# Kernel tuning notes

Hardware: AMD Instinct MI355X
Metric: run time of the kernel (lower is better)

Reference implementation:

```python
import jax, jax.numpy as jnp
import numpy as np

N_NODES = 100000
N_EDGES = 1600000
NUM_GRAPHS = 64
IN_CH, HID, NUM_CLASSES = 128, 64, 10


def _glorot(key, fan_in, fan_out):
    scale = jnp.sqrt(2.0 / (fan_in + fan_out)).astype(jnp.float32)
    return jax.random.normal(key, (fan_in, fan_out), jnp.float32) * scale


def setup_inputs() -> dict:
    key = jax.random.key(0)
    ks = jax.random.split(key, 7)
    x = jax.random.normal(ks[0], (N_NODES, IN_CH), jnp.float32)
    edge_index = jax.random.randint(ks[1], (2, N_EDGES), 0, N_NODES, dtype=jnp.int32)
    batch = jnp.sort(jax.random.randint(ks[2], (N_NODES,), 0, NUM_GRAPHS, dtype=jnp.int32))
    return {
        "x": x,
        "edge_index": edge_index,
        "batch": batch,
        "W1": _glorot(ks[3], IN_CH, HID), "b1": jnp.zeros((HID,), jnp.float32),
        "W2": _glorot(ks[4], HID, HID), "b2": jnp.zeros((HID,), jnp.float32),
        "W3": _glorot(ks[5], HID, NUM_CLASSES), "b3": jnp.zeros((NUM_CLASSES,), jnp.float32),
    }


def _gcn_conv(x, src, dst, norm, W, b):
    # GCNConv: h = X W, then symmetric-normalized scatter-add over edges, then + b
    h = x @ W                                  # [N, out]
    msg = norm[:, None] * h[src]               # [E+N, out] gather
    out = jax.ops.segment_sum(msg, dst, num_segments=N_NODES)
    return out + b


def reference(x, edge_index, batch, W1, b1, W2, b2, W3, b3):
    loop = jnp.arange(N_NODES, dtype=edge_index.dtype)
    src = jnp.concatenate([edge_index[0], loop])   # self-loops added (PyG gcn_norm)
    dst = jnp.concatenate([edge_index[1], loop])
    deg = jax.ops.segment_sum(jnp.ones(src.shape[0], x.dtype), dst, num_segments=N_NODES)
    dinv = jnp.where(deg > 0, jax.lax.rsqrt(deg), jnp.zeros_like(deg))
    norm = dinv[src] * dinv[dst]

    h = jax.nn.relu(_gcn_conv(x, src, dst, norm, W1, b1))  # dropout is identity in eval
    h = jax.nn.relu(_gcn_conv(h, src, dst, norm, W2, b2))
    h = _gcn_conv(h, src, dst, norm, W3, b3)

    counts = jax.ops.segment_sum(jnp.ones(N_NODES, h.dtype), batch, num_segments=NUM_GRAPHS)
    pooled = jax.ops.segment_sum(h, batch, num_segments=NUM_GRAPHS) / jnp.maximum(counts, 1.0)[:, None]
    return jax.nn.log_softmax(pooled, axis=1)
```

## Files before the change

### kernel.cpp

```cpp
#include <hip/hip_runtime.h>
#include <math.h>

#define IN_CH 128
#define HID   64
#define NC    10
#define BSH   8
#define NBLK  256

typedef unsigned short bfu;
typedef __attribute__((ext_vector_type(8))) short bf16x8;
typedef __attribute__((ext_vector_type(4))) float f32x4;
typedef __attribute__((ext_vector_type(2))) float f32x2;

static __device__ __forceinline__ bfu bf16_of(float f) {
    unsigned u = __float_as_uint(f);
    unsigned r = (u + 0x7FFF + ((u >> 16) & 1)) >> 16;
    return (bfu)r;
}

#if __has_builtin(__builtin_amdgcn_cvt_pk_f32_fp8) && __has_builtin(__builtin_amdgcn_cvt_pk_fp8_f32)
template <bool HI>
static __device__ __forceinline__ f32x2 fp8_unpk(unsigned d) {
    return __builtin_amdgcn_cvt_pk_f32_fp8((int)d, HI);
}
template <bool HI>
static __device__ __forceinline__ int fp8_pk(float a, float b, int old) {
    return __builtin_amdgcn_cvt_pk_fp8_f32(a, b, old, HI);
}
#else
static __device__ __forceinline__ float fp8_dec1(unsigned b) {
    unsigned s = b >> 7, e = (b >> 3) & 15, m = b & 7;
    float v = (e == 0) ? ldexpf((float)m, -9) : ldexpf((float)(8 + m), (int)e - 10);
    return s ? -v : v;
}
static __device__ __forceinline__ unsigned fp8_enc1(float f) {
    unsigned u = __float_as_uint(f);
    unsigned s = (u >> 31) << 7;
    f = fabsf(f);
    if (!(f < 448.f)) return s | 0x7E;
    if (f < 0.015625f) {
        int q = (int)rintf(f * 512.f);
        return s | (unsigned)q;
    }
    int e; float fr = frexpf(f, &e);
    int q = (int)rintf(fr * 16.f);
    if (q == 16) { q = 8; e++; }
    int E = e + 6;
    if (E >= 16) return s | 0x7E;
    return s | (unsigned)((E << 3) | (q - 8));
}
template <bool HI>
static __device__ __forceinline__ f32x2 fp8_unpk(unsigned d) {
    unsigned w = HI ? (d >> 16) : d;
    f32x2 r; r.x = fp8_dec1(w & 0xFF); r.y = fp8_dec1((w >> 8) & 0xFF);
    return r;
}
template <bool HI>
static __device__ __forceinline__ int fp8_pk(float a, float b, int old) {
    unsigned p = fp8_enc1(a) | (fp8_enc1(b) << 8);
    return HI ? (int)(((unsigned)old & 0x0000FFFFu) | (p << 16))
              : (int)(((unsigned)old & 0xFFFF0000u) | p);
}
#endif

__device__ __forceinline__ int lower_bound_i(const int* a, int n, int v) {
    int lo = 0, hi = n;
    while (lo < hi) { int mid = (lo + hi) >> 1; if (a[mid] < v) lo = mid + 1; else hi = mid; }
    return lo;
}


__global__ void k_init(int* __restrict__ cnt, float* __restrict__ Psum,
                       unsigned* __restrict__ dumA, unsigned* __restrict__ dumB,
                       const float* __restrict__ W1, const float* __restrict__ W2,
                       bfu* __restrict__ W1b, bfu* __restrict__ W2b,
                       int nbuck, int ng) {
    int t = threadIdx.x, b = blockIdx.x;
    if (b == 0) {
        for (int i = t; i < nbuck; i += 256) cnt[i] = 0;
        if (t < 16) { dumA[t] = 0u; dumB[t] = 0u; }
    } else if (b == 1) {
        for (int i = t; i < ng * HID; i += 256) Psum[i] = 0.f;
    } else if (b < 6) {
        int base = (b - 2) * 2048;
        for (int i = t; i < 2048; i += 256) {
            int idx = base + i;
            int k = idx >> 6, c = idx & 63;
            W1b[c * 136 + k] = bf16_of(W1[idx]);
        }
    } else {
        int base = (b - 6) * 2048;
        for (int i = t; i < 2048; i += 256) {
            int idx = base + i;
            int k = idx >> 6, c = idx & 63;
            W2b[c * 72 + k] = bf16_of(W2[idx]);
        }
    }
}


__global__ __launch_bounds__(1024) void k_part(const int* __restrict__ src,
                                               const int* __restrict__ dst,
                                               int* __restrict__ cnt,
                                               unsigned* __restrict__ packed,
                                               int E, int nbuck, int chunk, int cap) {
    __shared__ int hist[512];
    int tid = threadIdx.x;
    for (int b = tid; b < nbuck; b += 1024) hist[b] = 0;
    __syncthreads();
    int base = blockIdx.x * chunk;
    int lim  = min(base + chunk, E);
    for (int e = base + tid; e < lim; e += 1024)
        atomicAdd(&hist[dst[e] >> BSH], 1);
    __syncthreads();
    for (int b = tid; b < nbuck; b += 1024) {
        int c = hist[b];
        hist[b] = c ? atomicAdd(&cnt[b], c) : 0;
    }
    __syncthreads();
    for (int e = base + tid; e < lim; e += 1024) {
        int d = dst[e], s = src[e];
        int b = d >> BSH;
        int pos = atomicAdd(&hist[b], 1);
        if (pos < cap)
            packed[(size_t)b * (size_t)cap + pos] = ((unsigned)s << 8) | (unsigned)(d & 255);
    }
}


__global__ __launch_bounds__(1024) void k_placeC(const unsigned* __restrict__ packed,
                                                 const int* __restrict__ cnt,
                                                 int2* __restrict__ rp2,
                                                 float* __restrict__ dinv,
                                                 int* __restrict__ meta,
                                                 int nn, int cap, int capm) {
    __shared__ int hist[256];
    __shared__ int scn[256];
    __shared__ int cur[256];
    int tid = threadIdx.x;
    int b   = blockIdx.x;
    int nb0 = b << BSH;
    int nnb = min(1 << BSH, nn - nb0);
    if (tid < 256) hist[tid] = 0;
    __syncthreads();
    int lo = b * cap;
    int hi = lo + min(cnt[b], cap);
    for (int e = lo + tid; e < hi; e += blockDim.x)
        atomicAdd(&hist[packed[e] & 255u], 1);
    __syncthreads();
    int pd = 0;
    if (tid < 256) { pd = (hist[tid] + 3) & ~3; scn[tid] = pd; }
    __syncthreads();
    for (int off = 1; off < 256; off <<= 1) {
        int t = 0;
        if (tid < 256 && tid >= off) t = scn[tid - off];
        __syncthreads();
        if (tid < 256) scn[tid] += t;
        __syncthreads();
    }
    int meta0 = b * capm;
    if (tid < nnb) {
        int rp = meta0 + scn[tid] - pd;
        rp2[nb0 + tid] = make_int2(rp, rp + pd);
        cur[tid] = rp;
        dinv[nb0 + tid] = rsqrtf((float)(hist[tid] + 1));
        for (int k = hist[tid]; k < pd; k++) meta[rp + k] = nn;
    }
    __syncthreads();
    for (int e = lo + tid; e < hi; e += blockDim.x) {
        unsigned p = packed[e];
        int pos = atomicAdd(&cur[p & 255u], 1);
        meta[pos] = (int)(p >> 8);
    }
}


template <int K, bool IN_BF16>
__global__ __launch_bounds__(256) void k_gemm(const void* __restrict__ Xv,
                                              const bfu* __restrict__ Wb,
                                              const float* __restrict__ dinv,
                                              unsigned char* __restrict__ G8, int n) {
    constexpr int KS = K + 8;
    __shared__ bfu wt[64 * KS];
    int tid = threadIdx.x;
    {
        const uint4* wsrc = (const uint4*)Wb;
        uint4* wdst = (uint4*)wt;
        for (int i = tid; i < 8 * KS; i += 256) wdst[i] = wsrc[i];
    }
    __syncthreads();
    int wave = tid >> 6, lane = tid & 63;
    int m = lane & 15, q = lane >> 4;
    int row0 = blockIdx.x * 64 + wave * 16;
    int rowA = min(row0 + m, n - 1);
    f32x4 acc[4] = {{0.f,0.f,0.f,0.f},{0.f,0.f,0.f,0.f},
                    {0.f,0.f,0.f,0.f},{0.f,0.f,0.f,0.f}};
#pragma unroll
    for (int ks = 0; ks < K / 32; ks++) {
        bf16x8 a;
        if (IN_BF16) {
            a = *(const bf16x8*)((const bfu*)Xv + (size_t)rowA * 64 + ks * 32 + q * 8);
        } else {
            const float* xp = (const float*)Xv + (size_t)rowA * K + ks * 32 + q * 8;
            float4 v0 = *(const float4*)xp;
            float4 v1 = *(const float4*)(xp + 4);
            union { unsigned u[4]; bf16x8 v; } cvt;
            cvt.u[0] = __builtin_amdgcn_perm(__float_as_uint(v0.y), __float_as_uint(v0.x), 0x07060302u);
            cvt.u[1] = __builtin_amdgcn_perm(__float_as_uint(v0.w), __float_as_uint(v0.z), 0x07060302u);
            cvt.u[2] = __builtin_amdgcn_perm(__float_as_uint(v1.y), __float_as_uint(v1.x), 0x07060302u);
            cvt.u[3] = __builtin_amdgcn_perm(__float_as_uint(v1.w), __float_as_uint(v1.z), 0x07060302u);
            a = cvt.v;
        }
#pragma unroll
        for (int nt = 0; nt < 4; nt++) {
            bf16x8 b = *(const bf16x8*)&wt[(nt * 16 + m) * KS + ks * 32 + q * 8];
            acc[nt] = __builtin_amdgcn_mfma_f32_16x16x32_bf16(a, b, acc[nt], 0, 0, 0);
        }
    }
#pragma unroll
    for (int r = 0; r < 4; r++) {
        int grow = row0 + q * 4 + r;
        if (grow < n) {
            float dv = dinv[grow];
            int p01 = fp8_pk<false>(acc[0][r] * dv, acc[1][r] * dv, 0);
            int p23 = fp8_pk<false>(acc[2][r] * dv, acc[3][r] * dv, 0);
            unsigned char* gp = G8 + (size_t)grow * 64 + m;
            gp[0]  = (unsigned char)(p01 & 0xFF);
            gp[16] = (unsigned char)((p01 >> 8) & 0xFF);
            gp[32] = (unsigned char)(p23 & 0xFF);
            gp[48] = (unsigned char)((p23 >> 8) & 0xFF);
        }
    }
}


template <int MODE>
__global__ void k_agg(const unsigned* __restrict__ G4, const int* __restrict__ meta,
                      const int2* __restrict__ rp2, const float* __restrict__ dinv,
                      const float* __restrict__ bias, void* __restrict__ outv,
                      const int* __restrict__ batch, float* __restrict__ Psum,
                      const bfu* __restrict__ Wb,
                      int n, int ng, int do_relu, int post_scale) {
    extern __shared__ char smem[];
    int tid = threadIdx.x;
    if (MODE == 3) {
        bfu* wt = (bfu*)(smem + 16 * 72 * 2);
        const uint4* wsrc = (const uint4*)Wb;
        uint4* wdst = (uint4*)wt;
        for (int i = tid; i < 576; i += 256) wdst[i] = wsrc[i];
    }
    int wbase = ((blockIdx.x * blockDim.x + tid) >> 6) * 4;
    if (MODE == 1) { if (wbase >= n) return; }
    int lane = tid & 63;
    int col4 = lane & 15, equad = lane >> 4;
    int nb0 = blockIdx.x * 16;
    if (MODE == 2 && tid < 16) {
        int* sb = (int*)(smem + 16 * 64 * 4);
        sb[tid] = (nb0 + tid < n) ? batch[nb0 + tid] : -1;
    }
    int nd    = wbase + equad;
    bool alive = nd < n;
    int ndc   = alive ? nd : (n - 1);
    int2 rp = rp2[ndc];
    int beg = rp.x, pend = alive ? rp.y : rp.x;
    unsigned sv = G4[(size_t)ndc * 16 + col4];
    float dv = dinv[ndc];
    f32x2 aA = {0.f, 0.f}, aB = {0.f, 0.f};
    int e = beg;
    for (; e + 8 <= pend; e += 8) {
        int4 m0 = *(const int4*)&meta[e];
        int4 m1 = *(const int4*)&meta[e + 4];
        unsigned d0 = G4[(size_t)m0.x * 16 + col4];
        unsigned d1 = G4[(size_t)m0.y * 16 + col4];
        unsigned d2 = G4[(size_t)m0.z * 16 + col4];
        unsigned d3 = G4[(size_t)m0.w * 16 + col4];
        unsigned d4 = G4[(size_t)m1.x * 16 + col4];
        unsigned d5 = G4[(size_t)m1.y * 16 + col4];
        unsigned d6 = G4[(size_t)m1.z * 16 + col4];
        unsigned d7 = G4[(size_t)m1.w * 16 + col4];
        aA += fp8_unpk<false>(d0); aB += fp8_unpk<true>(d0);
        aA += fp8_unpk<false>(d1); aB += fp8_unpk<true>(d1);
        aA += fp8_unpk<false>(d2); aB += fp8_unpk<true>(d2);
        aA += fp8_unpk<false>(d3); aB += fp8_unpk<true>(d3);
        aA += fp8_unpk<false>(d4); aB += fp8_unpk<true>(d4);
        aA += fp8_unpk<false>(d5); aB += fp8_unpk<true>(d5);
        aA += fp8_unpk<false>(d6); aB += fp8_unpk<true>(d6);
        aA += fp8_unpk<false>(d7); aB += fp8_unpk<true>(d7);
    }
    if (e < pend) {
        int4 m = *(const int4*)&meta[e];
        unsigned d0 = G4[(size_t)m.x * 16 + col4];
        unsigned d1 = G4[(size_t)m.y * 16 + col4];
        unsigned d2 = G4[(size_t)m.z * 16 + col4];
        unsigned d3 = G4[(size_t)m.w * 16 + col4];
        aA += fp8_unpk<false>(d0); aB += fp8_unpk<true>(d0);
        aA += fp8_unpk<false>(d1); aB += fp8_unpk<true>(d1);
        aA += fp8_unpk<false>(d2); aB += fp8_unpk<true>(d2);
        aA += fp8_unpk<false>(d3); aB += fp8_unpk<true>(d3);
    }
    aA += fp8_unpk<false>(sv); aB += fp8_unpk<true>(sv);
    float a0 = aA.x * dv, a1 = aA.y * dv, a2 = aB.x * dv, a3 = aB.y * dv;
    if (bias) {
        float4 bv = *(const float4*)&bias[col4 * 4];
        a0 += bv.x; a1 += bv.y; a2 += bv.z; a3 += bv.w;
    }
    if (do_relu) {
        a0 = fmaxf(a0, 0.f); a1 = fmaxf(a1, 0.f);
        a2 = fmaxf(a2, 0.f); a3 = fmaxf(a3, 0.f);
    }
    if (post_scale) { a0 *= dv; a1 *= dv; a2 *= dv; a3 *= dv; }
    if (MODE == 3) {
        bfu* pw = (bfu*)smem;
        bfu* wt = (bfu*)(smem + 16 * 72 * 2);
        int slot = (tid >> 6) * 4 + equad;
        uint2 o;
        o.x = (unsigned)bf16_of(alive ? a0 : 0.f) | ((unsigned)bf16_of(alive ? a1 : 0.f) << 16);
        o.y = (unsigned)bf16_of(alive ? a2 : 0.f) | ((unsigned)bf16_of(alive ? a3 : 0.f) << 16);
        *(uint2*)&pw[slot * 72 + col4 * 4] = o;
        __syncthreads();
        int w = tid >> 6, m = col4, q = equad;
        f32x4 acc = {0.f, 0.f, 0.f, 0.f};
#pragma unroll
        for (int ks = 0; ks < 2; ks++) {
            bf16x8 av = *(const bf16x8*)&pw[m * 72 + ks * 32 + q * 8];
            bf16x8 bv = *(const bf16x8*)&wt[(w * 16 + m) * 72 + ks * 32 + q * 8];
            acc = __builtin_amdgcn_mfma_f32_16x16x32_bf16(av, bv, acc, 0, 0, 0);
        }
        int c = w * 16 + m;
        int r0 = nb0 + q * 4;
        float dv0 = dinv[min(r0 + 0, n - 1)], dv1 = dinv[min(r0 + 1, n - 1)];
        float dv2 = dinv[min(r0 + 2, n - 1)], dv3 = dinv[min(r0 + 3, n - 1)];
        int p01 = fp8_pk<false>(acc[0] * dv0, acc[1] * dv1, 0);
        int p23 = fp8_pk<false>(acc[2] * dv2, acc[3] * dv3, 0);
        unsigned char* gp = (unsigned char*)outv;
        if (r0 + 0 < n) gp[(size_t)(r0 + 0) * 64 + c] = (unsigned char)(p01 & 0xFF);
        if (r0 + 1 < n) gp[(size_t)(r0 + 1) * 64 + c] = (unsigned char)((p01 >> 8) & 0xFF);
        if (r0 + 2 < n) gp[(size_t)(r0 + 2) * 64 + c] = (unsigned char)(p23 & 0xFF);
        if (r0 + 3 < n) gp[(size_t)(r0 + 3) * 64 + c] = (unsigned char)((p23 >> 8) & 0xFF);
    } else if (MODE == 2) {
        float* pwf = (float*)smem;
        int*   sb  = (int*)(smem + 16 * 64 * 4);
        int slot = (tid >> 6) * 4 + equad;
        f32x4 st;
        st.x = alive ? a0 : 0.f; st.y = alive ? a1 : 0.f;
        st.z = alive ? a2 : 0.f; st.w = alive ? a3 : 0.f;
        *(f32x4*)&pwf[slot * 64 + col4 * 4] = st;
        __syncthreads();
        int r = tid >> 6, cc = tid & 63;
        int g0 = sb[0];
        float v = 0.f;
#pragma unroll
        for (int s2 = 0; s2 < 16; s2++)
            if (sb[s2] == g0 + r) v += pwf[s2 * 64 + cc];
        if (v != 0.f && g0 + r < ng) atomicAdd(&Psum[(g0 + r) * 64 + cc], v);
        if (tid < 16) {
            int bb = sb[tid];
            if (bb > g0 + 3) {
                for (int c2 = 0; c2 < 64; c2++)
                    atomicAdd(&Psum[bb * 64 + c2], pwf[tid * 64 + c2]);
            }
        }
    } else if (alive) {
        int p = fp8_pk<false>(a0, a1, 0);
        p = fp8_pk<true>(a2, a3, p);
        ((unsigned*)outv)[(size_t)nd * 16 + col4] = (unsigned)p;
    }
}


__global__ void k_final(const float* __restrict__ Psum, const int* __restrict__ batch,
                        int n, const float* __restrict__ W3, const float* __restrict__ b3,
                        float* __restrict__ out, int ng) {
    __shared__ float P[64 * 64];
    __shared__ float s[64][NC];
    __shared__ float lse[64];
    __shared__ float invc[64];
    int t = threadIdx.x;
    if (t < ng) {
        int lo = lower_bound_i(batch, n, t);
        int hi = lower_bound_i(batch, n, t + 1);
        invc[t] = 1.f / (float)max(hi - lo, 1);
    }
    __syncthreads();
    for (int i = t; i < ng * 64; i += blockDim.x) P[i] = Psum[i] * invc[i >> 6];
    __syncthreads();
    if (t < ng * NC) {
        int g = t / NC, c = t % NC;
        float acc = b3[c];
        for (int k = 0; k < 64; k++) acc += P[g * 64 + k] * W3[k * NC + c];
        s[g][c] = acc;
    }
    __syncthreads();
    if (t < ng) {
        float m = -1e30f;
        for (int c = 0; c < NC; c++) m = fmaxf(m, s[t][c]);
        float sum = 0.f;
        for (int c = 0; c < NC; c++) sum += expf(s[t][c] - m);
        lse[t] = m + logf(sum);
    }
    __syncthreads();
    if (t < ng * NC) {
        int g = t / NC, c = t % NC;
        out[t] = s[g][c] - lse[g];
    }
}


extern "C" void kernel_launch(void* const* d_in, const int* in_sizes, int n_in,
                              void* d_out, int out_size, void* d_ws, size_t ws_size,
                              hipStream_t stream) {
    const float* x     = (const float*)d_in[0];
    const int*   ei    = (const int*)  d_in[1];
    const int*   batch = (const int*)  d_in[2];
    const float* W1    = (const float*)d_in[3];
    const float* b1    = (const float*)d_in[4];
    const float* W2    = (const float*)d_in[5];
    const float* b2    = (const float*)d_in[6];
    const float* W3    = (const float*)d_in[7];
    const float* b3    = (const float*)d_in[8];
    float*       out   = (float*)d_out;

    const int NN = in_sizes[0] / IN_CH;
    const int E  = in_sizes[1] / 2;
    const int NG = out_size / NC;
    const int nbuck = (NN + (1 << BSH) - 1) >> BSH;
    const int cap   = (int)(((((long long)E << BSH) / NN) + 768 + 3) & ~3LL);
    const int capm  = cap + 772;

    const int* src = ei;
    const int* dst = ei + E;

    char* ws = (char*)d_ws;
    size_t off = 0;
    auto carve = [&](size_t bytes) -> char* {
        char* p = ws + off;
        off = (off + bytes + 255) & ~(size_t)255;
        return p;
    };
    int2*  rp2    = (int2*) carve((size_t)NN * 8);
    float* dinv   = (float*)carve((size_t)NN * 4);
    int*   cnt    = (int*)  carve((size_t)nbuck * 4);
    int*   meta   = (int*)  carve(((size_t)nbuck * capm + 64) * 4);
    unsigned char* f8A = (unsigned char*)carve((size_t)(NN + 1) * 64);
    unsigned char* f8B = (unsigned char*)carve((size_t)(NN + 1) * 64);
    unsigned* packed = (unsigned*)carve((size_t)nbuck * cap * 4);
    float* Psum   = (float*)carve((size_t)NG * HID * 4);
    bfu*   W1b    = (bfu*)  carve((size_t)64 * 136 * 2);
    bfu*   W2b    = (bfu*)  carve((size_t)64 * 72 * 2);
    (void)ws_size;

    const int chnk = (E + NBLK - 1) / NBLK;
    const int nbG  = (NN + 63) / 64;
    const int nbA  = (NN + 15) / 16;

    const int smem3 = (16 * 72 + 64 * 72) * 2;
    const int smem2 = 16 * 64 * 4 + 16 * 4;

    k_init<<<8, 256, 0, stream>>>(cnt, Psum,
                                  (unsigned*)(f8A + (size_t)NN * 64),
                                  (unsigned*)(f8B + (size_t)NN * 64),
                                  W1, W2, W1b, W2b, nbuck, NG);
    k_part<<<NBLK, 1024, 0, stream>>>(src, dst, cnt, packed, E, nbuck, chnk, cap);
    k_placeC<<<nbuck, 1024, 0, stream>>>(packed, cnt, rp2, dinv, meta, NN, cap, capm);

    k_gemm<IN_CH, false><<<nbG, 256, 0, stream>>>(x, W1b, dinv, f8A, NN);
    k_agg<3><<<nbA, 256, smem3, stream>>>((const unsigned*)f8A, meta, rp2, dinv, b1,
                                          f8B, nullptr, nullptr, W2b, NN, NG, 1, 0);
    k_agg<1><<<nbA, 256, 0, stream>>>((const unsigned*)f8B, meta, rp2, dinv, b2,
                                      f8A, nullptr, nullptr, nullptr, NN, NG, 1, 1);
    k_agg<2><<<nbA, 256, smem2, stream>>>((const unsigned*)f8A, meta, rp2, dinv, nullptr,
                                          nullptr, batch, Psum, nullptr, NN, NG, 0, 0);
    k_final<<<1, 640, 0, stream>>>(Psum, batch, NN, W3, b3, out, NG);
}
```

Before: 232.5 us.

## Count degrees in partition pass and fuse final pooling head into last aggregation

Per-node in-degrees are now counted with global atomics during the edge partition pass, so the placement kernel no longer makes a separate histogram pass over the packed edges. The standalone final kernel is removed. Its work (mean pooling, the W3 projection and log_softmax) now runs in the last block of the final aggregation kernel, chosen with a completion counter and a thread fence, which saves one launch. The cost is 1.6M extra global atomics on random addresses in the partition pass, plus a larger shared-memory footprint for the last aggregation kernel.

```diff
diff --git a/kernel.cpp b/kernel.cpp
--- a/kernel.cpp
+++ b/kernel.cpp
@@ -74,10 +74,11 @@
                        unsigned* __restrict__ dumA, unsigned* __restrict__ dumB,
                        const float* __restrict__ W1, const float* __restrict__ W2,
                        bfu* __restrict__ W1b, bfu* __restrict__ W2b,
-                       int nbuck, int ng) {
+                       int* __restrict__ deg, int nn, int nbuck, int ng) {
     int t = threadIdx.x, b = blockIdx.x;
+    for (int i = b * 256 + t; i < nn; i += 8 * 256) deg[i] = 0;
     if (b == 0) {
-        for (int i = t; i < nbuck; i += 256) cnt[i] = 0;
+        for (int i = t; i < nbuck + 1; i += 256) cnt[i] = 0;
         if (t < 16) { dumA[t] = 0u; dumB[t] = 0u; }
     } else if (b == 1) {
         for (int i = t; i < ng * HID; i += 256) Psum[i] = 0.f;
@@ -102,6 +103,7 @@
 __global__ __launch_bounds__(1024) void k_part(const int* __restrict__ src,
                                                const int* __restrict__ dst,
                                                int* __restrict__ cnt,
+                                               int* __restrict__ deg,
                                                unsigned* __restrict__ packed,
                                                int E, int nbuck, int chunk, int cap) {
     __shared__ int hist[512];
@@ -110,8 +112,11 @@
     __syncthreads();
     int base = blockIdx.x * chunk;
     int lim  = min(base + chunk, E);
-    for (int e = base + tid; e < lim; e += 1024)
-        atomicAdd(&hist[dst[e] >> BSH], 1);
+    for (int e = base + tid; e < lim; e += 1024) {
+        int d = dst[e];
+        atomicAdd(&hist[d >> BSH], 1);
+        atomicAdd(&deg[d], 1);
+    }
     __syncthreads();
     for (int b = tid; b < nbuck; b += 1024) {
         int c = hist[b];
@@ -130,26 +135,23 @@
 
 __global__ __launch_bounds__(1024) void k_placeC(const unsigned* __restrict__ packed,
                                                  const int* __restrict__ cnt,
+                                                 const int* __restrict__ deg,
                                                  int2* __restrict__ rp2,
                                                  float* __restrict__ dinv,
                                                  int* __restrict__ meta,
                                                  int nn, int cap, int capm) {
-    __shared__ int hist[256];
     __shared__ int scn[256];
     __shared__ int cur[256];
     int tid = threadIdx.x;
     int b   = blockIdx.x;
     int nb0 = b << BSH;
     int nnb = min(1 << BSH, nn - nb0);
-    if (tid < 256) hist[tid] = 0;
-    __syncthreads();
-    int lo = b * cap;
-    int hi = lo + min(cnt[b], cap);
-    for (int e = lo + tid; e < hi; e += blockDim.x)
-        atomicAdd(&hist[packed[e] & 255u], 1);
-    __syncthreads();
-    int pd = 0;
-    if (tid < 256) { pd = (hist[tid] + 3) & ~3; scn[tid] = pd; }
+    int dg = 0, pd = 0;
+    if (tid < 256) {
+        dg = (tid < nnb) ? deg[nb0 + tid] : 0;
+        pd = (dg + 3) & ~3;
+        scn[tid] = pd;
+    }
     __syncthreads();
     for (int off = 1; off < 256; off <<= 1) {
         int t = 0;
@@ -163,10 +165,12 @@
         int rp = meta0 + scn[tid] - pd;
         rp2[nb0 + tid] = make_int2(rp, rp + pd);
         cur[tid] = rp;
-        dinv[nb0 + tid] = rsqrtf((float)(hist[tid] + 1));
-        for (int k = hist[tid]; k < pd; k++) meta[rp + k] = nn;
-    }
-    __syncthreads();
+        dinv[nb0 + tid] = rsqrtf((float)(dg + 1));
+        for (int k = dg; k < pd; k++) meta[rp + k] = nn;
+    }
+    __syncthreads();
+    int lo = b * cap;
+    int hi = lo + min(cnt[b], cap);
     for (int e = lo + tid; e < hi; e += blockDim.x) {
         unsigned p = packed[e];
         int pos = atomicAdd(&cur[p & 255u], 1);
@@ -240,6 +244,8 @@
                       const float* __restrict__ bias, void* __restrict__ outv,
                       const int* __restrict__ batch, float* __restrict__ Psum,
                       const bfu* __restrict__ Wb,
+                      const float* __restrict__ W3, const float* __restrict__ b3,
+                      float* __restrict__ outp, int* __restrict__ donecnt,
                       int n, int ng, int do_relu, int post_scale) {
     extern __shared__ char smem[];
     int tid = threadIdx.x;
@@ -255,7 +261,7 @@
     int col4 = lane & 15, equad = lane >> 4;
     int nb0 = blockIdx.x * 16;
     if (MODE == 2 && tid < 16) {
-        int* sb = (int*)(smem + 16 * 64 * 4);
+        int* sb = (int*)(smem + 19456);
         sb[tid] = (nb0 + tid < n) ? batch[nb0 + tid] : -1;
     }
     int nd    = wbase + equad;
@@ -339,7 +345,7 @@
         if (r0 + 3 < n) gp[(size_t)(r0 + 3) * 64 + c] = (unsigned char)((p23 >> 8) & 0xFF);
     } else if (MODE == 2) {
         float* pwf = (float*)smem;
-        int*   sb  = (int*)(smem + 16 * 64 * 4);
+        int*   sb  = (int*)(smem + 19456);
         int slot = (tid >> 6) * 4 + equad;
         f32x4 st;
         st.x = alive ? a0 : 0.f; st.y = alive ? a1 : 0.f;
@@ -360,48 +366,50 @@
                     atomicAdd(&Psum[bb * 64 + c2], pwf[tid * 64 + c2]);
             }
         }
+        __threadfence();
+        __shared__ int lastf;
+        if (tid == 0) {
+            int rk = atomicAdd(donecnt, 1);
+            lastf = (rk == (int)gridDim.x - 1) ? 1 : 0;
+        }
+        __syncthreads();
+        if (lastf) {
+            float* P    = (float*)smem;
+            float* sS   = (float*)(smem + 16384);
+            float* lse  = (float*)(smem + 18944);
+            float* invc = (float*)(smem + 19200);
+            if (tid < ng) {
+                int lo2 = lower_bound_i(batch, n, tid);
+                int hi2 = lower_bound_i(batch, n, tid + 1);
+                invc[tid] = 1.f / (float)max(hi2 - lo2, 1);
+            }
+            __syncthreads();
+            for (int i = tid; i < ng * 64; i += 256)
+                P[i] = __hip_atomic_load(&Psum[i], __ATOMIC_RELAXED,
+                                         __HIP_MEMORY_SCOPE_AGENT) * invc[i >> 6];
+            __syncthreads();
+            for (int idx = tid; idx < ng * NC; idx += 256) {
+                int g = idx / NC, c = idx % NC;
+                float acc2 = b3[c];
+                for (int k = 0; k < 64; k++) acc2 += P[g * 64 + k] * W3[k * NC + c];
+                sS[idx] = acc2;
+            }
+            __syncthreads();
+            if (tid < ng) {
+                float mx = -1e30f;
+                for (int c = 0; c < NC; c++) mx = fmaxf(mx, sS[tid * NC + c]);
+                float sum = 0.f;
+                for (int c = 0; c < NC; c++) sum += expf(sS[tid * NC + c] - mx);
+                lse[tid] = mx + logf(sum);
+            }
+            __syncthreads();
+            for (int idx = tid; idx < ng * NC; idx += 256)
+                outp[idx] = sS[idx] - lse[idx / NC];
+        }
     } else if (alive) {
         int p = fp8_pk<false>(a0, a1, 0);
         p = fp8_pk<true>(a2, a3, p);
         ((unsigned*)outv)[(size_t)nd * 16 + col4] = (unsigned)p;
-    }
-}
-
-
-__global__ void k_final(const float* __restrict__ Psum, const int* __restrict__ batch,
-                        int n, const float* __restrict__ W3, const float* __restrict__ b3,
-                        float* __restrict__ out, int ng) {
-    __shared__ float P[64 * 64];
-    __shared__ float s[64][NC];
-    __shared__ float lse[64];
-    __shared__ float invc[64];
-    int t = threadIdx.x;
-    if (t < ng) {
-        int lo = lower_bound_i(batch, n, t);
-        int hi = lower_bound_i(batch, n, t + 1);
-        invc[t] = 1.f / (float)max(hi - lo, 1);
-    }
-    __syncthreads();
-    for (int i = t; i < ng * 64; i += blockDim.x) P[i] = Psum[i] * invc[i >> 6];
-    __syncthreads();
-    if (t < ng * NC) {
-        int g = t / NC, c = t % NC;
-        float acc = b3[c];
-        for (int k = 0; k < 64; k++) acc += P[g * 64 + k] * W3[k * NC + c];
-        s[g][c] = acc;
-    }
-    __syncthreads();
-    if (t < ng) {
-        float m = -1e30f;
-        for (int c = 0; c < NC; c++) m = fmaxf(m, s[t][c]);
-        float sum = 0.f;
-        for (int c = 0; c < NC; c++) sum += expf(s[t][c] - m);
-        lse[t] = m + logf(sum);
-    }
-    __syncthreads();
-    if (t < ng * NC) {
-        int g = t / NC, c = t % NC;
-        out[t] = s[g][c] - lse[g];
     }
 }
 
@@ -439,7 +447,8 @@
     };
     int2*  rp2    = (int2*) carve((size_t)NN * 8);
     float* dinv   = (float*)carve((size_t)NN * 4);
-    int*   cnt    = (int*)  carve((size_t)nbuck * 4);
+    int*   cnt    = (int*)  carve((size_t)(nbuck + 1) * 4);
+    int*   deg    = (int*)  carve((size_t)NN * 4);
     int*   meta   = (int*)  carve(((size_t)nbuck * capm + 64) * 4);
     unsigned char* f8A = (unsigned char*)carve((size_t)(NN + 1) * 64);
     unsigned char* f8B = (unsigned char*)carve((size_t)(NN + 1) * 64);
@@ -448,27 +457,30 @@
     bfu*   W1b    = (bfu*)  carve((size_t)64 * 136 * 2);
     bfu*   W2b    = (bfu*)  carve((size_t)64 * 72 * 2);
     (void)ws_size;
+    int* donecnt = cnt + nbuck;
 
     const int chnk = (E + NBLK - 1) / NBLK;
     const int nbG  = (NN + 63) / 64;
     const int nbA  = (NN + 15) / 16;
 
     const int smem3 = (16 * 72 + 64 * 72) * 2;
-    const int smem2 = 16 * 64 * 4 + 16 * 4;
+    const int smem2 = 19520;
 
     k_init<<<8, 256, 0, stream>>>(cnt, Psum,
                                   (unsigned*)(f8A + (size_t)NN * 64),
                                   (unsigned*)(f8B + (size_t)NN * 64),
-                                  W1, W2, W1b, W2b, nbuck, NG);
-    k_part<<<NBLK, 1024, 0, stream>>>(src, dst, cnt, packed, E, nbuck, chnk, cap);
-    k_placeC<<<nbuck, 1024, 0, stream>>>(packed, cnt, rp2, dinv, meta, NN, cap, capm);
+                                  W1, W2, W1b, W2b, deg, NN, nbuck, NG);
+    k_part<<<NBLK, 1024, 0, stream>>>(src, dst, cnt, deg, packed, E, nbuck, chnk, cap);
+    k_placeC<<<nbuck, 1024, 0, stream>>>(packed, cnt, deg, rp2, dinv, meta, NN, cap, capm);
 
     k_gemm<IN_CH, false><<<nbG, 256, 0, stream>>>(x, W1b, dinv, f8A, NN);
     k_agg<3><<<nbA, 256, smem3, stream>>>((const unsigned*)f8A, meta, rp2, dinv, b1,
-                                          f8B, nullptr, nullptr, W2b, NN, NG, 1, 0);
+                                          f8B, nullptr, nullptr, W2b,
+                                          nullptr, nullptr, nullptr, nullptr, NN, NG, 1, 0);
     k_agg<1><<<nbA, 256, 0, stream>>>((const unsigned*)f8B, meta, rp2, dinv, b2,
-                                      f8A, nullptr, nullptr, nullptr, NN, NG, 1, 1);
+                                      f8A, nullptr, nullptr, nullptr,
+                                      nullptr, nullptr, nullptr, nullptr, NN, NG, 1, 1);
     k_agg<2><<<nbA, 256, smem2, stream>>>((const unsigned*)f8A, meta, rp2, dinv, nullptr,
-                                          nullptr, batch, Psum, nullptr, NN, NG, 0, 0);
-    k_final<<<1, 640, 0, stream>>>(Psum, batch, NN, W3, b3, out, NG);
-}
+                                          nullptr, batch, Psum, nullptr,
+                                          W3, b3, out, donecnt, NN, NG, 0, 0);
+}
```

Result: slower. 688.2 us (+196.1%).

## Reorder aggregation nodes by in-degree within buckets for wave load balance

Applied to the files above, without the earlier changes.

Within each 256-node bucket, nodes are counting-sorted by in-degree into an order array. The aggregation kernels for layers 1 and 2 then process nodes in that order, so the four nodes a wavefront handles have similar edge counts and less lane divergence. Output stores are scattered to the permuted row indices, and the MFMA epilogue now writes single bytes per row through the indirection. The costs are the extra sort work in placement, one extra indirect load per node, and less coalesced writes.

```diff
diff --git a/kernel.cpp b/kernel.cpp
--- a/kernel.cpp
+++ b/kernel.cpp
@@ -133,15 +133,19 @@
                                                  int2* __restrict__ rp2,
                                                  float* __restrict__ dinv,
                                                  int* __restrict__ meta,
+                                                 int* __restrict__ order,
                                                  int nn, int cap, int capm) {
     __shared__ int hist[256];
     __shared__ int scn[256];
     __shared__ int cur[256];
+    __shared__ int bins[64];
+    __shared__ int bcur[64];
     int tid = threadIdx.x;
     int b   = blockIdx.x;
     int nb0 = b << BSH;
     int nnb = min(1 << BSH, nn - nb0);
     if (tid < 256) hist[tid] = 0;
+    if (tid >= 256 && tid < 320) bins[tid - 256] = 0;
     __syncthreads();
     int lo = b * cap;
     int hi = lo + min(cnt[b], cap);
@@ -159,12 +163,27 @@
         __syncthreads();
     }
     int meta0 = b * capm;
+    int dgc = 0;
     if (tid < nnb) {
         int rp = meta0 + scn[tid] - pd;
         rp2[nb0 + tid] = make_int2(rp, rp + pd);
         cur[tid] = rp;
         dinv[nb0 + tid] = rsqrtf((float)(hist[tid] + 1));
         for (int k = hist[tid]; k < pd; k++) meta[rp + k] = nn;
+        dgc = min(hist[tid], 63);
+        atomicAdd(&bins[dgc], 1);
+    }
+    __syncthreads();
+    if (tid == 0) {
+        int run = 0;
+        for (int i = 0; i < 64; i++) { int t = bins[i]; bins[i] = run; run += t; }
+    }
+    __syncthreads();
+    if (tid < 64) bcur[tid] = bins[tid];
+    __syncthreads();
+    if (tid < nnb) {
+        int rk = atomicAdd(&bcur[dgc], 1);
+        order[nb0 + rk] = nb0 + tid;
     }
     __syncthreads();
     for (int e = lo + tid; e < hi; e += blockDim.x) {
@@ -239,7 +258,7 @@
                       const int2* __restrict__ rp2, const float* __restrict__ dinv,
                       const float* __restrict__ bias, void* __restrict__ outv,
                       const int* __restrict__ batch, float* __restrict__ Psum,
-                      const bfu* __restrict__ Wb,
+                      const bfu* __restrict__ Wb, const int* __restrict__ order,
                       int n, int ng, int do_relu, int post_scale) {
     extern __shared__ char smem[];
     int tid = threadIdx.x;
@@ -258,9 +277,11 @@
         int* sb = (int*)(smem + 16 * 64 * 4);
         sb[tid] = (nb0 + tid < n) ? batch[nb0 + tid] : -1;
     }
-    int nd    = wbase + equad;
-    bool alive = nd < n;
-    int ndc   = alive ? nd : (n - 1);
+    int pos   = wbase + equad;
+    bool alive = pos < n;
+    int ndc;
+    if (MODE == 2) ndc = alive ? pos : (n - 1);
+    else           ndc = order[alive ? pos : (n - 1)];
     int2 rp = rp2[ndc];
     int beg = rp.x, pend = alive ? rp.y : rp.x;
     unsigned sv = G4[(size_t)ndc * 16 + col4];
@@ -327,16 +348,15 @@
             acc = __builtin_amdgcn_mfma_f32_16x16x32_bf16(av, bv, acc, 0, 0, 0);
         }
         int c = w * 16 + m;
-        int r0 = nb0 + q * 4;
-        float dv0 = dinv[min(r0 + 0, n - 1)], dv1 = dinv[min(r0 + 1, n - 1)];
-        float dv2 = dinv[min(r0 + 2, n - 1)], dv3 = dinv[min(r0 + 3, n - 1)];
-        int p01 = fp8_pk<false>(acc[0] * dv0, acc[1] * dv1, 0);
-        int p23 = fp8_pk<false>(acc[2] * dv2, acc[3] * dv3, 0);
         unsigned char* gp = (unsigned char*)outv;
-        if (r0 + 0 < n) gp[(size_t)(r0 + 0) * 64 + c] = (unsigned char)(p01 & 0xFF);
-        if (r0 + 1 < n) gp[(size_t)(r0 + 1) * 64 + c] = (unsigned char)((p01 >> 8) & 0xFF);
-        if (r0 + 2 < n) gp[(size_t)(r0 + 2) * 64 + c] = (unsigned char)(p23 & 0xFF);
-        if (r0 + 3 < n) gp[(size_t)(r0 + 3) * 64 + c] = (unsigned char)((p23 >> 8) & 0xFF);
+#pragma unroll
+        for (int r = 0; r < 4; r++) {
+            int pr = nb0 + q * 4 + r;
+            int row = order[min(pr, n - 1)];
+            float dvr = dinv[row];
+            unsigned p8 = (unsigned)fp8_pk<false>(acc[r] * dvr, 0.f, 0) & 0xFFu;
+            if (pr < n) gp[(size_t)row * 64 + c] = (unsigned char)p8;
+        }
     } else if (MODE == 2) {
         float* pwf = (float*)smem;
         int*   sb  = (int*)(smem + 16 * 64 * 4);
@@ -363,7 +383,7 @@
     } else if (alive) {
         int p = fp8_pk<false>(a0, a1, 0);
         p = fp8_pk<true>(a2, a3, p);
-        ((unsigned*)outv)[(size_t)nd * 16 + col4] = (unsigned)p;
+        ((unsigned*)outv)[(size_t)ndc * 16 + col4] = (unsigned)p;
     }
 }
 
@@ -440,6 +460,7 @@
     int2*  rp2    = (int2*) carve((size_t)NN * 8);
     float* dinv   = (float*)carve((size_t)NN * 4);
     int*   cnt    = (int*)  carve((size_t)nbuck * 4);
+    int*   order  = (int*)  carve((size_t)NN * 4);
     int*   meta   = (int*)  carve(((size_t)nbuck * capm + 64) * 4);
     unsigned char* f8A = (unsigned char*)carve((size_t)(NN + 1) * 64);
     unsigned char* f8B = (unsigned char*)carve((size_t)(NN + 1) * 64);
@@ -461,14 +482,18 @@
                                   (unsigned*)(f8B + (size_t)NN * 64),
                                   W1, W2, W1b, W2b, nbuck, NG);
     k_part<<<NBLK, 1024, 0, stream>>>(src, dst, cnt, packed, E, nbuck, chnk, cap);
-    k_placeC<<<nbuck, 1024, 0, stream>>>(packed, cnt, rp2, dinv, meta, NN, cap, capm);
+    k_placeC<<<nbuck, 1024, 0, stream>>>(packed, cnt, rp2, dinv, meta, order,
+                                         NN, cap, capm);
 
     k_gemm<IN_CH, false><<<nbG, 256, 0, stream>>>(x, W1b, dinv, f8A, NN);
     k_agg<3><<<nbA, 256, smem3, stream>>>((const unsigned*)f8A, meta, rp2, dinv, b1,
-                                          f8B, nullptr, nullptr, W2b, NN, NG, 1, 0);
+                                          f8B, nullptr, nullptr, W2b, order,
+                                          NN, NG, 1, 0);
     k_agg<1><<<nbA, 256, 0, stream>>>((const unsigned*)f8B, meta, rp2, dinv, b2,
-                                      f8A, nullptr, nullptr, nullptr, NN, NG, 1, 1);
+                                      f8A, nullptr, nullptr, nullptr, order,
+                                      NN, NG, 1, 1);
     k_agg<2><<<nbA, 256, smem2, stream>>>((const unsigned*)f8A, meta, rp2, dinv, nullptr,
-                                          nullptr, batch, Psum, nullptr, NN, NG, 0, 0);
+                                          nullptr, batch, Psum, nullptr, nullptr,
+                                          NN, NG, 0, 0);
     k_final<<<1, 640, 0, stream>>>(Psum, batch, NN, W3, b3, out, NG);
 }
```

New measurement: 245.9 us. +5.8%, slower.
